# Kernel tuning notes

Hardware: AMD Instinct MI355X
Metric: run time of the kernel (lower is better)

## Reference

```python
import jax, jax.numpy as jnp
import numpy as np

NU, NI, E, D, B, L = 100000, 50000, 800000, 64, 1024, 2
P_DROP, TEMP = 0.25, 0.2
L1, L2, L3 = 0.2, 0.01, 1e-5


def setup_inputs() -> dict:
    k = jax.random.split(jax.random.key(0), 20)
    s = 0.02  # xavier-ish scale for embedding tables
    return dict(
        E_u_0=jax.random.normal(k[0], (NU, D), jnp.float32) * s,
        E_i_0=jax.random.normal(k[1], (NI, D), jnp.float32) * s,
        fuse_w=jax.random.normal(k[2], (E,), jnp.float32),
        fuse_b=jax.random.normal(k[3], (E,), jnp.float32),
        W1u=jax.random.normal(k[4], (D, D), jnp.float32) / np.sqrt(D),
        W1i=jax.random.normal(k[5], (D, D), jnp.float32) / np.sqrt(D),
        b1=jnp.zeros((D,), jnp.float32),
        W2=jax.random.normal(k[6], (D,), jnp.float32) / np.sqrt(D),
        b2=jnp.zeros((1,), jnp.float32),
        att_a=jax.random.normal(k[7], (2 * D,), jnp.float32) / np.sqrt(2 * D),
        wv_param=jax.random.normal(k[8], (E,), jnp.float32),
        Wg=jax.random.normal(k[9], (D, D), jnp.float32) / np.sqrt(D),
        adj_vals=jax.random.uniform(k[10], (E,), jnp.float32, 0.001, 0.02),
        drop_main_u=jax.random.uniform(k[11], (2 * L, E), jnp.float32),
        drop_aug_u=jax.random.uniform(k[12], (2 * L, E), jnp.float32),
        edge_src=jax.random.randint(k[13], (E,), 0, NU),
        edge_dst=jax.random.randint(k[14], (E,), 0, NI),
        uids=jax.random.randint(k[15], (B,), 0, NU),
        iids=jax.random.randint(k[16], (B,), 0, NI),
        pos_ids=jax.random.randint(k[17], (B,), 0, NI),
        neg_ids=jax.random.randint(k[18], (B,), 0, NI),
    )


def _forward(E_u_0, E_i_0, fuse_w, fuse_b, W1u, W1i, b1, W2, b2, att_a,
             wv_param, Wg, adj_vals, drop_main_u, drop_aug_u,
             edge_src, edge_dst, uids, iids, pos_ids, neg_ids):
    dt = adj_vals.dtype

    def spmm_u(vals, Xi):  # A @ Xi -> [NU, D]
        return jax.ops.segment_sum(vals[:, None] * Xi[edge_dst], edge_src, num_segments=NU)

    def spmm_i(vals, Xu):  # A.T @ Xu -> [NI, D]
        return jax.ops.segment_sum(vals[:, None] * Xu[edge_src], edge_dst, num_segments=NI)

    def mask(u):  # sparse_dropout: keep w.p. 1-p, rescale
        return (u > P_DROP).astype(dt) / (1.0 - P_DROP)

    def propagate(vals, drops):  # LightGCN-style sum over layers
        Eu, Ei = E_u_0, E_i_0
        Su, Si = Eu, Ei
        for layer in range(L):
            Eu_n = spmm_u(vals * mask(drops[2 * layer]), Ei)
            Ei_n = spmm_i(vals * mask(drops[2 * layer + 1]), Eu)
            Eu, Ei = Eu_n, Ei_n
            Su, Si = Su + Eu, Si + Ei
        return Su, Si

    E_u, E_i = propagate(adj_vals, drop_main_u)

    eu0, ei0 = E_u_0[edge_src], E_i_0[edge_dst]  # [E, D]
    # MLP view
    h = jax.nn.relu(eu0 @ W1u + ei0 @ W1i + b1)
    Ag_mlp = jax.nn.sigmoid(h @ W2 + b2[0])
    # WV view: learnable per-edge weight
    Ag_wv = jax.nn.sigmoid(wv_param)
    # GCN view: one propagation on current embeddings, bilinear edge score
    h_u = spmm_u(adj_vals, E_i)
    h_i = spmm_i(adj_vals, E_u)
    Ag_gcn = jax.nn.sigmoid(jnp.sum((h_u[edge_src] @ Wg) * h_i[edge_dst], axis=1))
    # ATT view: GAT-style
    Ag_att = jax.nn.sigmoid(jax.nn.leaky_relu(eu0 @ att_a[:D] + ei0 @ att_a[D:], 0.2))

    views = jnp.stack([Ag_mlp, Ag_wv, Ag_gcn, Ag_att])  # [4, E]
    w = jax.nn.softmax(jnp.tanh(fuse_w * views + fuse_b), axis=1)  # softmax over edges (as in source)
    Ag = jnp.sum(w * views, axis=0)
    Ag = (Ag + (views - Ag).sum(0)) / 5.0  # mlp_cof = 1 -> (sum(views) - 3*Ag) / 5

    # refine: sigmoid of endpoint dot products
    pre = jax.nn.sigmoid(jnp.sum(E_u[edge_src] * E_i[edge_dst], axis=1))
    baew = pre * Ag  # batch_aug_edge_weight

    aug_vals = jax.lax.stop_gradient(baew) * adj_vals  # new_graph * adj_norm (detach + Hadamard)
    Z_u, Z_i = propagate(aug_vals, drop_aug_u)

    # contrastive loss
    Gu, Gi = Z_u[uids], Z_i[iids]
    neg_sc = jnp.log(jnp.exp(Gu @ E_u.T / TEMP).sum(1) + 1e-8).mean() \
           + jnp.log(jnp.exp(Gi @ E_i.T / TEMP).sum(1) + 1e-8).mean()
    pos_sc = jnp.clip((Gu * E_u[uids]).sum(1) / TEMP, -5.0, 5.0).mean() \
           + jnp.clip((Gi * E_i[iids]).sum(1) / TEMP, -5.0, 5.0).mean()
    loss_cl = -pos_sc + neg_sc

    # BPR loss
    u_e, p_e, n_e = E_u[uids], E_i[pos_ids], E_i[neg_ids]
    diff = (u_e * p_e).sum(-1) - (u_e * n_e).sum(-1)
    loss_bpr = -jnp.log(jax.nn.sigmoid(diff)).mean()

    loss_pr = L2 * (-jnp.log(baew)).mean()

    params = [E_u_0, E_i_0, fuse_w, fuse_b, W1u, W1i, b1, W2, b2, att_a, wv_param, Wg]
    loss_reg = L3 * sum((p_ ** 2).sum() for p_ in params)

    loss = loss_bpr + L1 * loss_cl + loss_pr + loss_reg
    return loss, loss_bpr, L1 * loss_cl, loss_pr


def reference(E_u_0, E_i_0, fuse_w, fuse_b, W1u, W1i, b1, W2, b2, att_a,
              wv_param, Wg, adj_vals, drop_main_u, drop_aug_u,
              edge_src, edge_dst, uids, iids, pos_ids, neg_ids):
    return _forward(E_u_0, E_i_0, fuse_w, fuse_b, W1u, W1i, b1, W2, b2, att_a,
                    wv_param, Wg, adj_vals, drop_main_u, drop_aug_u,
                    edge_src, edge_dst, uids, iids, pos_ids, neg_ids)
```

## Files before the change

### kernel.cpp

```cpp
#include <hip/hip_runtime.h>
#include <math.h>

constexpr int NUc = 100000;
constexpr int NIc = 50000;
constexpr int Ec  = 800000;
constexpr int Bc  = 1024;

typedef __attribute__((ext_vector_type(8))) short short8;
typedef __attribute__((ext_vector_type(8))) unsigned short ushort8;
typedef __attribute__((ext_vector_type(4))) unsigned short ushort4v;
typedef __attribute__((ext_vector_type(4))) float floatx4;

__device__ __forceinline__ float sigf(float x) { return 1.f / (1.f + __expf(-x)); }
__device__ __forceinline__ float maskf(float u) { return (u > 0.25f) ? (1.f / 0.75f) : 0.f; }
__device__ __forceinline__ unsigned short f2bf(float f) {
    unsigned int u = __float_as_uint(f);
    unsigned int r = (u + 0x7fffu + ((u >> 16) & 1u)) >> 16;
    return (unsigned short)r;
}
__device__ __forceinline__ float bf2f(unsigned short u) {
    return __uint_as_float((unsigned int)u << 16);
}

__global__ void hist_k(const int* __restrict__ idx, int* __restrict__ cnt, int n) {
    int i = blockIdx.x * blockDim.x + threadIdx.x;
    if (i < n) atomicAdd(&cnt[idx[i]], 1);
}

__global__ void scan_block(const int* __restrict__ cnt, int* __restrict__ rp,
                           int* __restrict__ bsum, int N) {
    __shared__ int sh[1024];
    int i = blockIdx.x * 1024 + threadIdx.x;
    int v = (i < N) ? cnt[i] : 0;
    sh[threadIdx.x] = v;
    __syncthreads();
    for (int off = 1; off < 1024; off <<= 1) {
        int t = (threadIdx.x >= off) ? sh[threadIdx.x - off] : 0;
        __syncthreads();
        sh[threadIdx.x] += t;
        __syncthreads();
    }
    if (i < N) rp[i + 1] = sh[threadIdx.x];
    if (threadIdx.x == 1023) bsum[blockIdx.x] = sh[1023];
}

__global__ void scan_bsums(int* __restrict__ bsum, int nb) {
    __shared__ int sh[128];
    int t = threadIdx.x;
    int v = (t < nb) ? bsum[t] : 0;
    sh[t] = v;
    __syncthreads();
    for (int off = 1; off < 128; off <<= 1) {
        int x = (t >= off) ? sh[t - off] : 0;
        __syncthreads();
        sh[t] += x;
        __syncthreads();
    }
    if (t < nb) bsum[t] = sh[t] - v;
}

__global__ void scan_add(const int* __restrict__ bsum, int* __restrict__ rp, int N) {
    int i = blockIdx.x * blockDim.x + threadIdx.x;
    if (i == 0) rp[0] = 0;
    if (i < N) rp[i + 1] += bsum[i >> 10];
}

__global__ void fill_csr(const int* __restrict__ key, const int* __restrict__ other,
                         const float* __restrict__ adj, int* __restrict__ cur,
                         int* __restrict__ col, float* __restrict__ adjP,
                         int* __restrict__ pos, int n) {
    int i = blockIdx.x * blockDim.x + threadIdx.x;
    if (i < n) {
        int r = key[i];
        int p = atomicAdd(&cur[r], 1);
        col[p] = other[i];
        adjP[p] = adj[i];
        pos[i] = p;
    }
}

__global__ void build_rowu(const int* __restrict__ rp, int* __restrict__ rowu, int N) {
    int r = blockIdx.x * blockDim.x + threadIdx.x;
    if (r < N) {
        int s = rp[r], e = rp[r + 1];
        for (int p = s; p < e; ++p) rowu[p] = r;
    }
}

__global__ void build_wmain(const int* __restrict__ posu, const int* __restrict__ posi,
                            const float* __restrict__ adj, const float* __restrict__ dmain,
                            float* __restrict__ wMu0, float* __restrict__ wMu1,
                            float* __restrict__ wMi0, float* __restrict__ wMi1, int E) {
    int e = blockIdx.x * blockDim.x + threadIdx.x;
    if (e >= E) return;
    float a = adj[e];
    int pu = posu[e], pi = posi[e];
    wMu0[pu] = a * maskf(dmain[e]);
    wMi0[pi] = a * maskf(dmain[(size_t)Ec + e]);
    wMu1[pu] = a * maskf(dmain[2 * (size_t)Ec + e]);
    wMi1[pi] = a * maskf(dmain[3 * (size_t)Ec + e]);
}

__global__ void spmm_bf(const int* __restrict__ rp, const int* __restrict__ col,
                        const float* __restrict__ w, const unsigned short* __restrict__ Xbf,
                        float* __restrict__ Acc, const float* __restrict__ Base,
                        unsigned short* __restrict__ Ybf, int ystride, int yoff, int N) {
    int row = blockIdx.x * (blockDim.x >> 6) + (threadIdx.x >> 6);
    int lane = threadIdx.x & 63;
    if (row >= N) return;
    int s = rp[row], e = rp[row + 1];
    float acc = 0.f;
    int j = s;
    for (; j + 4 <= e; j += 4) {
        int c0 = col[j], c1 = col[j + 1], c2 = col[j + 2], c3 = col[j + 3];
        float w0 = w[j], w1 = w[j + 1], w2 = w[j + 2], w3 = w[j + 3];
        float x0 = bf2f(Xbf[(size_t)c0 * 64 + lane]);
        float x1 = bf2f(Xbf[(size_t)c1 * 64 + lane]);
        float x2 = bf2f(Xbf[(size_t)c2 * 64 + lane]);
        float x3 = bf2f(Xbf[(size_t)c3 * 64 + lane]);
        acc = fmaf(w0, x0, acc);
        acc = fmaf(w1, x1, acc);
        acc = fmaf(w2, x2, acc);
        acc = fmaf(w3, x3, acc);
    }
    for (; j < e; ++j) acc = fmaf(w[j], bf2f(Xbf[(size_t)col[j] * 64 + lane]), acc);
    size_t o = (size_t)row * 64 + lane;
    if (Acc) Acc[o] = (Base ? Base[o] : Acc[o]) + acc;
    if (Ybf) Ybf[(size_t)row * ystride + yoff + lane] = f2bf(acc);
}

__global__ void gemm_n64_bf(const unsigned short* __restrict__ Xbf, const float* __restrict__ W,
                            unsigned short* __restrict__ P, int ostride, int ooff, int N) {
    __shared__ float Wl[64 * 64];
    for (int i = threadIdx.x; i < 4096; i += blockDim.x) Wl[i] = W[i];
    __syncthreads();
    int wid = blockIdx.x * (blockDim.x >> 6) + (threadIdx.x >> 6);
    int lane = threadIdx.x & 63;
    for (int r = 0; r < 8; ++r) {
        int row = wid * 8 + r;
        if (row >= N) break;
        const unsigned short* xr = Xbf + (size_t)row * 64;
        float acc = 0.f;
#pragma unroll
        for (int k = 0; k < 64; ++k) acc = fmaf(bf2f(xr[k]), Wl[k * 64 + lane], acc);
        P[(size_t)row * ostride + ooff + lane] = f2bf(acc);
    }
}

__global__ void rowdot64(const float* __restrict__ X, const float* __restrict__ a,
                         float* __restrict__ out, int N) {
    int wid = blockIdx.x * (blockDim.x >> 6) + (threadIdx.x >> 6);
    int lane = threadIdx.x & 63;
    float av = a[lane];
    for (int r = 0; r < 8; ++r) {
        int row = wid * 8 + r;
        if (row >= N) break;
        float v = X[(size_t)row * 64 + lane] * av;
#pragma unroll
        for (int off = 32; off; off >>= 1) v += __shfl_xor(v, off, 64);
        if (lane == 0) out[row] = v;
    }
}

__global__ void cvt_bf16(const float4* __restrict__ X, ushort4* __restrict__ Y, int n4) {
    int i = blockIdx.x * blockDim.x + threadIdx.x;
    if (i < n4) {
        float4 v = X[i];
        Y[i] = make_ushort4(f2bf(v.x), f2bf(v.y), f2bf(v.z), f2bf(v.w));
    }
}

__global__ void cvt_pack4(const float4* __restrict__ X, unsigned short* __restrict__ P,
                          int ostride, int ooff, int N) {
    int t = blockIdx.x * blockDim.x + threadIdx.x;
    if (t >= N * 16) return;
    int node = t >> 4, q = t & 15;
    float4 v = X[t];
    ushort4* dst = (ushort4*)(P + (size_t)node * ostride + ooff);
    dst[q] = make_ushort4(f2bf(v.x), f2bf(v.y), f2bf(v.z), f2bf(v.w));
}

__global__ void pack_bf4(const ushort4* __restrict__ X, unsigned short* __restrict__ P,
                         int ostride, int ooff, int N) {
    int t = blockIdx.x * blockDim.x + threadIdx.x;
    if (t >= N * 16) return;
    int node = t >> 4, q = t & 15;
    ((ushort4*)(P + (size_t)node * ostride + ooff))[q] = X[t];
}

__global__ void __launch_bounds__(128) edge_pass1(
        const int* __restrict__ rowu, const int* __restrict__ colP,
        const unsigned short* __restrict__ PU, const unsigned short* __restrict__ PI,
        const float* __restrict__ b1, const float* __restrict__ W2,
        const float* __restrict__ b2,
        const float* __restrict__ auv, const float* __restrict__ aiv,
        float4* __restrict__ vp4, int E) {
    __shared__ ushort4v lds4[128 * 49];
    int p0 = blockIdx.x * 128;
    int tid = threadIdx.x;
#pragma unroll
    for (int it = 0; it < 24; ++it) {
        int flat = it * 128 + tid;
        int row = flat / 24, c = flat - row * 24;
        int d = colP[p0 + row];
        ushort8 g = *(const ushort8*)(PI + (size_t)d * 192 + c * 8);
        ushort4v lo = {g[0], g[1], g[2], g[3]};
        ushort4v hi = {g[4], g[5], g[6], g[7]};
        lds4[row * 49 + c * 2]     = lo;
        lds4[row * 49 + c * 2 + 1] = hi;
    }
    __syncthreads();
    int p = p0 + tid;
    int s = rowu[p];
    int d = colP[p];
    const ushort8* pu = (const ushort8*)(PU + (size_t)s * 192);
    const ushort4v* pl = lds4 + tid * 49;
    float r1 = 0.f, r2 = 0.f, r3 = 0.f;
#pragma unroll
    for (int k = 0; k < 8; ++k) {
        ushort8 u1 = pu[k], hu = pu[8 + k], su = pu[16 + k];
        ushort4v i1a = pl[2 * k], i1b = pl[2 * k + 1];
        ushort4v hia = pl[16 + 2 * k], hib = pl[16 + 2 * k + 1];
        ushort4v sia = pl[32 + 2 * k], sib = pl[32 + 2 * k + 1];
#pragma unroll
        for (int j = 0; j < 4; ++j) {
            float h = bf2f(u1[j]) + bf2f(i1a[j]) + b1[k * 8 + j];
            r1 = fmaf(fmaxf(h, 0.f), W2[k * 8 + j], r1);
            r2 = fmaf(bf2f(hu[j]), bf2f(hia[j]), r2);
            r3 = fmaf(bf2f(su[j]), bf2f(sia[j]), r3);
        }
#pragma unroll
        for (int j = 0; j < 4; ++j) {
            float h = bf2f(u1[4 + j]) + bf2f(i1b[j]) + b1[k * 8 + 4 + j];
            r1 = fmaf(fmaxf(h, 0.f), W2[k * 8 + 4 + j], r1);
            r2 = fmaf(bf2f(hu[4 + j]), bf2f(hib[j]), r2);
            r3 = fmaf(bf2f(su[4 + j]), bf2f(sib[j]), r3);
        }
    }
    float v0 = sigf(r1 + b2[0]);
    float v2 = sigf(r2);
    float ax = auv[s] + aiv[d];
    float v3 = sigf(ax > 0.f ? ax : 0.2f * ax);
    float pre = sigf(r3);
    vp4[p] = make_float4(v0, v2, v3, pre);
}

__global__ void edge_pass2a(const float4* __restrict__ vp4, const int* __restrict__ posu,
                            const float* __restrict__ fw, const float* __restrict__ fb,
                            const float* __restrict__ wv,
                            float4* __restrict__ viewsE, float* __restrict__ preE,
                            float* __restrict__ sumexp, int E) {
    int e = blockIdx.x * blockDim.x + threadIdx.x;
    float ex0 = 0.f, ex1 = 0.f, ex2 = 0.f, ex3 = 0.f;
    if (e < E) {
        float4 t = vp4[posu[e]];
        float v0 = t.x, v2 = t.y, v3 = t.z;
        float v1 = sigf(wv[e]);
        viewsE[e] = make_float4(v0, v1, v2, v3);
        preE[e] = t.w;
        float fwe = fw[e], fbe = fb[e];
        ex0 = __expf(tanhf(fmaf(fwe, v0, fbe)));
        ex1 = __expf(tanhf(fmaf(fwe, v1, fbe)));
        ex2 = __expf(tanhf(fmaf(fwe, v2, fbe)));
        ex3 = __expf(tanhf(fmaf(fwe, v3, fbe)));
    }
#pragma unroll
    for (int off = 32; off; off >>= 1) {
        ex0 += __shfl_xor(ex0, off, 64);
        ex1 += __shfl_xor(ex1, off, 64);
        ex2 += __shfl_xor(ex2, off, 64);
        ex3 += __shfl_xor(ex3, off, 64);
    }
    __shared__ float sh[4][4];
    int w = threadIdx.x >> 6;
    if ((threadIdx.x & 63) == 0) {
        sh[w][0] = ex0; sh[w][1] = ex1; sh[w][2] = ex2; sh[w][3] = ex3;
    }
    __syncthreads();
    if (threadIdx.x < 4)
        atomicAdd(&sumexp[threadIdx.x],
                  sh[0][threadIdx.x] + sh[1][threadIdx.x] + sh[2][threadIdx.x] + sh[3][threadIdx.x]);
}

__global__ void edge_pass2b(const float4* __restrict__ viewsE, const float* __restrict__ preE,
                            const float* __restrict__ fw, const float* __restrict__ fb,
                            const float* __restrict__ adj, const float* __restrict__ daug,
                            const int* __restrict__ posu, const int* __restrict__ posi,
                            const float* __restrict__ sumexp,
                            float* __restrict__ wAu0, float* __restrict__ wAu1,
                            float* __restrict__ wAi0, float* __restrict__ wAi1,
                            float* __restrict__ neglog, int E) {
    int e = blockIdx.x * blockDim.x + threadIdx.x;
    float nl = 0.f;
    if (e < E) {
        float s0 = sumexp[0], s1 = sumexp[1], s2 = sumexp[2], s3 = sumexp[3];
        float4 v = viewsE[e];
        float fwe = fw[e], fbe = fb[e];
        float w0 = __expf(tanhf(fmaf(fwe, v.x, fbe))) / s0;
        float w1 = __expf(tanhf(fmaf(fwe, v.y, fbe))) / s1;
        float w2 = __expf(tanhf(fmaf(fwe, v.z, fbe))) / s2;
        float w3 = __expf(tanhf(fmaf(fwe, v.w, fbe))) / s3;
        float agw = w0 * v.x + w1 * v.y + w2 * v.z + w3 * v.w;
        float sv = v.x + v.y + v.z + v.w;
        float Ag = (sv - 3.f * agw) * 0.2f;
        float bw = preE[e] * Ag;
        float av = bw * adj[e];
        int pu = posu[e], pi = posi[e];
        wAu0[pu] = av * maskf(daug[e]);
        wAi0[pi] = av * maskf(daug[(size_t)Ec + e]);
        wAu1[pu] = av * maskf(daug[2 * (size_t)Ec + e]);
        wAi1[pi] = av * maskf(daug[3 * (size_t)Ec + e]);
        nl = -logf(bw);
    }
#pragma unroll
    for (int off = 32; off; off >>= 1) nl += __shfl_xor(nl, off, 64);
    __shared__ float sh4[4];
    if ((threadIdx.x & 63) == 0) sh4[threadIdx.x >> 6] = nl;
    __syncthreads();
    if (threadIdx.x == 0) atomicAdd(neglog, sh4[0] + sh4[1] + sh4[2] + sh4[3]);
}

__global__ void gather_cvt(const float* __restrict__ X, const int* __restrict__ ids,
                           unsigned short* __restrict__ Y, int B_) {
    int t = blockIdx.x * blockDim.x + threadIdx.x;
    if (t >= B_ * 64) return;
    int b = t >> 6, k = t & 63;
    Y[t] = f2bf(X[(size_t)ids[b] * 64 + k]);
}

__global__ void lse_mfma(const unsigned short* __restrict__ Gbf,
                         const unsigned short* __restrict__ Ebf,
                         float* __restrict__ sums, int N, int tilesPerChunk) {
    int wid = blockIdx.x * (blockDim.x >> 6) + (threadIdx.x >> 6);
    int lane = threadIdx.x & 63;
    int bgroup = wid & 15;
    int chunk = wid >> 4;
    int ntiles = N >> 4;
    int t0 = chunk * tilesPerChunk;
    if (t0 >= ntiles) return;
    int t1 = t0 + tilesPerChunk; if (t1 > ntiles) t1 = ntiles;
    int m = lane & 15, quad = lane >> 4;

    short8 a0[4], a1[4];
#pragma unroll
    for (int t = 0; t < 4; ++t) {
        const short8* ap = (const short8*)(Gbf + ((size_t)(bgroup * 64 + t * 16 + m)) * 64 + quad * 8);
        a0[t] = ap[0];
        a1[t] = ap[4];
    }
    floatx4 rs[4];
#pragma unroll
    for (int t = 0; t < 4; ++t) rs[t] = (floatx4){0.f, 0.f, 0.f, 0.f};

    for (int jt = t0; jt < t1; ++jt) {
        const short8* bp = (const short8*)(Ebf + ((size_t)(jt * 16 + m)) * 64 + quad * 8);
        short8 bf0 = bp[0], bf1 = bp[4];
#pragma unroll
        for (int t = 0; t < 4; ++t) {
            floatx4 c = (floatx4){0.f, 0.f, 0.f, 0.f};
            c = __builtin_amdgcn_mfma_f32_16x16x32_bf16(a0[t], bf0, c, 0, 0, 0);
            c = __builtin_amdgcn_mfma_f32_16x16x32_bf16(a1[t], bf1, c, 0, 0, 0);
#pragma unroll
            for (int r = 0; r < 4; ++r) rs[t][r] += __expf(c[r] * 5.f);
        }
    }
#pragma unroll
    for (int t = 0; t < 4; ++t) {
#pragma unroll
        for (int r = 0; r < 4; ++r) {
            float v = rs[t][r];
            v += __shfl_xor(v, 1, 64);
            v += __shfl_xor(v, 2, 64);
            v += __shfl_xor(v, 4, 64);
            v += __shfl_xor(v, 8, 64);
            if (m == 0) atomicAdd(&sums[bgroup * 64 + t * 16 + quad * 4 + r], v);
        }
    }
}

__global__ void sumsq(const float* __restrict__ x, int n, float* __restrict__ acc) {
    float s = 0.f;
    for (int i = blockIdx.x * blockDim.x + threadIdx.x; i < n; i += gridDim.x * blockDim.x) {
        float v = x[i];
        s = fmaf(v, v, s);
    }
#pragma unroll
    for (int off = 32; off; off >>= 1) s += __shfl_xor(s, off, 64);
    __shared__ float sh[4];
    if ((threadIdx.x & 63) == 0) sh[threadIdx.x >> 6] = s;
    __syncthreads();
    if (threadIdx.x == 0) atomicAdd(acc, sh[0] + sh[1] + sh[2] + sh[3]);
}

__global__ void finalize_kernel(const float* __restrict__ sumexp_u, const float* __restrict__ sumexp_i,
                                const float* __restrict__ Su, const float* __restrict__ Si,
                                const float* __restrict__ Zu, const float* __restrict__ Zi,
                                const int* __restrict__ uids, const int* __restrict__ iids,
                                const int* __restrict__ pids, const int* __restrict__ nids,
                                const float* __restrict__ neglog, const float* __restrict__ regsum,
                                float* __restrict__ out) {
    int b = threadIdx.x;
    float lse = logf(sumexp_u[b] + 1e-8f) + logf(sumexp_i[b] + 1e-8f);
    int u = uids[b], ii = iids[b], p = pids[b], n = nids[b];
    const float* zu = Zu + (size_t)u * 64;
    const float* su = Su + (size_t)u * 64;
    const float* zi = Zi + (size_t)ii * 64;
    const float* si = Si + (size_t)ii * 64;
    const float* pe = Si + (size_t)p * 64;
    const float* ne = Si + (size_t)n * 64;
    float du = 0.f, di = 0.f, dp = 0.f, dn = 0.f;
#pragma unroll
    for (int k = 0; k < 64; ++k) {
        du = fmaf(zu[k], su[k], du);
        di = fmaf(zi[k], si[k], di);
        dp = fmaf(su[k], pe[k], dp);
        dn = fmaf(su[k], ne[k], dn);
    }
    float pos = fminf(fmaxf(du * 5.f, -5.f), 5.f) + fminf(fmaxf(di * 5.f, -5.f), 5.f);
    float diff = dp - dn;
    float bpr = log1pf(__expf(-diff));
#pragma unroll
    for (int off = 32; off; off >>= 1) {
        lse += __shfl_xor(lse, off, 64);
        pos += __shfl_xor(pos, off, 64);
        bpr += __shfl_xor(bpr, off, 64);
    }
    __shared__ float sl[16], sp[16], sb[16];
    int w = b >> 6;
    if ((b & 63) == 0) { sl[w] = lse; sp[w] = pos; sb[w] = bpr; }
    __syncthreads();
    if (b == 0) {
        float L = 0.f, P = 0.f, Bz = 0.f;
        for (int i = 0; i < 16; ++i) { L += sl[i]; P += sp[i]; Bz += sb[i]; }
        float neg_sc = L * (1.f / Bc);
        float pos_sc = P * (1.f / Bc);
        float loss_cl = neg_sc - pos_sc;
        float l1cl = 0.2f * loss_cl;
        float loss_bpr = Bz * (1.f / Bc);
        float loss_pr = 0.01f * (neglog[0] * (1.f / Ec));
        float loss_reg = 1e-5f * regsum[0];
        out[0] = loss_bpr + l1cl + loss_pr + loss_reg;
        out[1] = loss_bpr;
        out[2] = l1cl;
        out[3] = loss_pr;
    }
}

extern "C" void kernel_launch(void* const* d_in, const int* in_sizes, int n_in,
                              void* d_out, int out_size, void* d_ws, size_t ws_size,
                              hipStream_t stream) {
    const float* Eu0    = (const float*)d_in[0];
    const float* Ei0    = (const float*)d_in[1];
    const float* fuse_w = (const float*)d_in[2];
    const float* fuse_b = (const float*)d_in[3];
    const float* W1u    = (const float*)d_in[4];
    const float* W1i    = (const float*)d_in[5];
    const float* b1     = (const float*)d_in[6];
    const float* W2     = (const float*)d_in[7];
    const float* b2     = (const float*)d_in[8];
    const float* att    = (const float*)d_in[9];
    const float* wv     = (const float*)d_in[10];
    const float* Wg     = (const float*)d_in[11];
    const float* adj    = (const float*)d_in[12];
    const float* dmain  = (const float*)d_in[13];
    const float* daug   = (const float*)d_in[14];
    const int*   esrc   = (const int*)d_in[15];
    const int*   edst   = (const int*)d_in[16];
    const int*   uids   = (const int*)d_in[17];
    const int*   iids   = (const int*)d_in[18];
    const int*   pids   = (const int*)d_in[19];
    const int*   nids   = (const int*)d_in[20];
    float* out = (float*)d_out;

    char* base = (char*)d_ws;
    size_t off = 0;
    auto alloc = [&](size_t bytes) -> char* {
        char* pp = base + off;
        off = (off + bytes + 255) & ~(size_t)255;
        return pp;
    };
    float* Su   = (float*)alloc((size_t)NUc * 64 * 4);
    float* Si   = (float*)alloc((size_t)NIc * 64 * 4);
    char* blkZ = alloc((size_t)NUc * 64 * 4 + (size_t)NIc * 64 * 4);
    unsigned short* PU = (unsigned short*)blkZ;
    float4* viewsE = (float4*)blkZ;
    float* preE   = (float*)(blkZ + (size_t)Ec * 16);
    float* Zu = (float*)blkZ;
    float* Zi = (float*)(blkZ + (size_t)NUc * 64 * 4);
    float4* vp4 = (float4*)alloc((size_t)Ec * 16);
    unsigned short* Eu0bf = (unsigned short*)alloc((size_t)NUc * 64 * 2);
    unsigned short* Ei0bf = (unsigned short*)alloc((size_t)NIc * 64 * 2);
    unsigned short* Subf  = (unsigned short*)alloc((size_t)NUc * 64 * 2);
    unsigned short* Sibf  = (unsigned short*)alloc((size_t)NIc * 64 * 2);
    unsigned short* Bubf  = (unsigned short*)alloc((size_t)NUc * 64 * 2);
    unsigned short* Bibf  = (unsigned short*)alloc((size_t)NIc * 64 * 2);
    unsigned short* hubf  = (unsigned short*)alloc((size_t)NUc * 64 * 2);
    unsigned short* hibf  = (unsigned short*)alloc((size_t)NIc * 64 * 2);
    char* blkA = alloc((size_t)Ec * 4 * 6);
    float* adjPu = (float*)blkA;
    float* adjPi = (float*)(blkA + (size_t)Ec * 4);
    float* wAu0  = (float*)(blkA + (size_t)Ec * 8);
    float* wAu1  = (float*)(blkA + (size_t)Ec * 12);
    float* wAi0  = (float*)(blkA + (size_t)Ec * 16);
    float* wAi1  = (float*)(blkA + (size_t)Ec * 20);
    unsigned short* PI = (unsigned short*)blkA;
    float* wMu0  = (float*)alloc((size_t)Ec * 4);
    float* wMu1  = (float*)alloc((size_t)Ec * 4);
    float* wMi0  = (float*)alloc((size_t)Ec * 4);
    float* wMi1  = (float*)alloc((size_t)Ec * 4);
    float* auv  = (float*)alloc((size_t)NUc * 4);
    float* aiv  = (float*)alloc((size_t)NIc * 4);
    int* rowu  = (int*)alloc((size_t)Ec * 4);
    unsigned short* Gubf = (unsigned short*)alloc((size_t)Bc * 64 * 2);
    unsigned short* Gibf = (unsigned short*)alloc((size_t)Bc * 64 * 2);
    float* sumexp4 = (float*)alloc(4 * 4);
    float* neglog  = (float*)alloc(4);
    float* regsum  = (float*)alloc(4);
    float* sumexp_u= (float*)alloc((size_t)Bc * 4);
    float* sumexp_i= (float*)alloc((size_t)Bc * 4);
    int* rpu   = (int*)alloc((size_t)(NUc + 1) * 4);
    int* rpi   = (int*)alloc((size_t)(NIc + 1) * 4);
    int* colu  = (int*)alloc((size_t)Ec * 4);
    int* coli  = (int*)alloc((size_t)Ec * 4);
    int* posu  = (int*)alloc((size_t)Ec * 4);
    int* posi  = (int*)alloc((size_t)Ec * 4);
    int* cnt   = (int*)alloc((size_t)NUc * 4);
    int* cur   = (int*)alloc((size_t)NUc * 4);
    int* bsum  = (int*)alloc(128 * 4);

    dim3 b256(256);
    const int nbU = (NUc + 1023) / 1024;
    const int nbI = (NIc + 1023) / 1024;
    const dim3 gE((Ec + 255) / 256);
    const dim3 gU((NUc + 3) / 4), gI((NIc + 3) / 4);
    const dim3 gU8((NUc + 31) / 32), gI8((NIc + 31) / 32);
    const dim3 gUp((NUc * 16 + 255) / 256), gIp((NIc * 16 + 255) / 256);

    hipMemsetAsync(cnt, 0, (size_t)NUc * 4, stream);
    hist_k<<<gE, b256, 0, stream>>>(esrc, cnt, Ec);
    scan_block<<<dim3(nbU), dim3(1024), 0, stream>>>(cnt, rpu, bsum, NUc);
    scan_bsums<<<dim3(1), dim3(128), 0, stream>>>(bsum, nbU);
    scan_add<<<dim3((NUc + 255) / 256), b256, 0, stream>>>(bsum, rpu, NUc);
    hipMemcpyAsync(cur, rpu, (size_t)NUc * 4, hipMemcpyDeviceToDevice, stream);
    fill_csr<<<gE, b256, 0, stream>>>(esrc, edst, adj, cur, colu, adjPu, posu, Ec);
    build_rowu<<<dim3((NUc + 255) / 256), b256, 0, stream>>>(rpu, rowu, NUc);

    hipMemsetAsync(cnt, 0, (size_t)NIc * 4, stream);
    hist_k<<<gE, b256, 0, stream>>>(edst, cnt, Ec);
    scan_block<<<dim3(nbI), dim3(1024), 0, stream>>>(cnt, rpi, bsum, NIc);
    scan_bsums<<<dim3(1), dim3(128), 0, stream>>>(bsum, nbI);
    scan_add<<<dim3((NIc + 255) / 256), b256, 0, stream>>>(bsum, rpi, NIc);
    hipMemcpyAsync(cur, rpi, (size_t)NIc * 4, hipMemcpyDeviceToDevice, stream);
    fill_csr<<<gE, b256, 0, stream>>>(edst, esrc, adj, cur, coli, adjPi, posi, Ec);

    build_wmain<<<gE, b256, 0, stream>>>(posu, posi, adj, dmain, wMu0, wMu1, wMi0, wMi1, Ec);

    cvt_bf16<<<gUp, b256, 0, stream>>>((const float4*)Eu0, (ushort4*)Eu0bf, NUc * 16);
    cvt_bf16<<<gIp, b256, 0, stream>>>((const float4*)Ei0, (ushort4*)Ei0bf, NIc * 16);

    spmm_bf<<<gU, b256, 0, stream>>>(rpu, colu, wMu0, Ei0bf, Su, Eu0, Bubf, 64, 0, NUc);
    spmm_bf<<<gI, b256, 0, stream>>>(rpi, coli, wMi0, Eu0bf, Si, Ei0, Bibf, 64, 0, NIc);
    spmm_bf<<<gU, b256, 0, stream>>>(rpu, colu, wMu1, Bibf, Su, nullptr, nullptr, 64, 0, NUc);
    spmm_bf<<<gI, b256, 0, stream>>>(rpi, coli, wMi1, Bubf, Si, nullptr, nullptr, 64, 0, NIc);

    cvt_bf16<<<gUp, b256, 0, stream>>>((const float4*)Su, (ushort4*)Subf, NUc * 16);
    cvt_bf16<<<gIp, b256, 0, stream>>>((const float4*)Si, (ushort4*)Sibf, NIc * 16);

    spmm_bf<<<gU, b256, 0, stream>>>(rpu, colu, adjPu, Sibf, nullptr, nullptr, hubf, 64, 0, NUc);
    spmm_bf<<<gI, b256, 0, stream>>>(rpi, coli, adjPi, Subf, nullptr, nullptr, hibf, 64, 0, NIc);
    gemm_n64_bf<<<gU8, b256, 0, stream>>>(hubf, Wg, PU, 192, 64, NUc);
    gemm_n64_bf<<<gU8, b256, 0, stream>>>(Eu0bf, W1u, PU, 192, 0, NUc);
    gemm_n64_bf<<<gI8, b256, 0, stream>>>(Ei0bf, W1i, PI, 192, 0, NIc);
    pack_bf4<<<gIp, b256, 0, stream>>>((const ushort4*)hibf, PI, 192, 64, NIc);
    cvt_pack4<<<gUp, b256, 0, stream>>>((const float4*)Su, PU, 192, 128, NUc);
    cvt_pack4<<<gIp, b256, 0, stream>>>((const float4*)Si, PI, 192, 128, NIc);

    rowdot64<<<gU8, b256, 0, stream>>>(Eu0, att, auv, NUc);
    rowdot64<<<gI8, b256, 0, stream>>>(Ei0, att + 64, aiv, NIc);

    edge_pass1<<<dim3(Ec / 128), dim3(128), 0, stream>>>(
        rowu, colu, PU, PI, b1, W2, b2, auv, aiv, vp4, Ec);

    hipMemsetAsync(sumexp4, 0, 4 * 4, stream);
    edge_pass2a<<<gE, b256, 0, stream>>>(vp4, posu, fuse_w, fuse_b, wv,
                                         viewsE, preE, sumexp4, Ec);

    hipMemsetAsync(neglog, 0, 4, stream);
    edge_pass2b<<<gE, b256, 0, stream>>>(
        viewsE, preE, fuse_w, fuse_b, adj, daug, posu, posi, sumexp4,
        wAu0, wAu1, wAi0, wAi1, neglog, Ec);

    spmm_bf<<<gU, b256, 0, stream>>>(rpu, colu, wAu0, Ei0bf, Zu, Eu0, Bubf, 64, 0, NUc);
    spmm_bf<<<gI, b256, 0, stream>>>(rpi, coli, wAi0, Eu0bf, Zi, Ei0, Bibf, 64, 0, NIc);
    spmm_bf<<<gU, b256, 0, stream>>>(rpu, colu, wAu1, Bibf, Zu, nullptr, nullptr, 64, 0, NUc);
    spmm_bf<<<gI, b256, 0, stream>>>(rpi, coli, wAi1, Bubf, Zi, nullptr, nullptr, 64, 0, NIc);

    gather_cvt<<<dim3((Bc * 64 + 255) / 256), b256, 0, stream>>>(Zu, uids, Gubf, Bc);
    gather_cvt<<<dim3((Bc * 64 + 255) / 256), b256, 0, stream>>>(Zi, iids, Gibf, Bc);
    hipMemsetAsync(sumexp_u, 0, (size_t)Bc * 4, stream);
    hipMemsetAsync(sumexp_i, 0, (size_t)Bc * 4, stream);
    lse_mfma<<<dim3(640), b256, 0, stream>>>(Gubf, Subf, sumexp_u, NUc, 40);
    lse_mfma<<<dim3(320), b256, 0, stream>>>(Gibf, Sibf, sumexp_i, NIc, 40);

    hipMemsetAsync(regsum, 0, 4, stream);
    auto ss = [&](const float* p, int n) {
        int g = (n + 2047) / 2048;
        if (g > 1024) g = 1024;
        if (g < 1) g = 1;
        sumsq<<<dim3(g), b256, 0, stream>>>(p, n, regsum);
    };
    ss(Eu0, NUc * 64); ss(Ei0, NIc * 64); ss(fuse_w, Ec); ss(fuse_b, Ec);
    ss(W1u, 4096); ss(W1i, 4096); ss(b1, 64); ss(W2, 64); ss(b2, 1);
    ss(att, 128); ss(wv, Ec); ss(Wg, 4096);

    finalize_kernel<<<dim3(1), dim3(1024), 0, stream>>>(
        sumexp_u, sumexp_i, Su, Si, Zu, Zi, uids, iids, pids, nids, neglog, regsum, out);
}
```

Before: 1.390 ms.

## Replace scattered edge-weight writes with permutation gathers and parallelize batch dot products

The CSR fill now records a permutation from CSR position to original edge. Main and augmented edge-weight arrays are built by gathering through that permutation, so the old random scatter writes via posu/posi become coalesced writes with random reads. The batch dot products formerly done serially per thread in the single-block finalize kernel move to a wave-per-sample kernel with shuffle reductions. This adds extra kernel launches, an extra intermediate array and some re-reading of the mask arrays.

```diff
diff --git a/kernel.cpp b/kernel.cpp
--- a/kernel.cpp
+++ b/kernel.cpp
@@ -66,16 +66,15 @@
 }
 
 __global__ void fill_csr(const int* __restrict__ key, const int* __restrict__ other,
-                         const float* __restrict__ adj, int* __restrict__ cur,
-                         int* __restrict__ col, float* __restrict__ adjP,
-                         int* __restrict__ pos, int n) {
+                         int* __restrict__ cur, int* __restrict__ col,
+                         int* __restrict__ pos, int* __restrict__ perm, int n) {
     int i = blockIdx.x * blockDim.x + threadIdx.x;
     if (i < n) {
         int r = key[i];
         int p = atomicAdd(&cur[r], 1);
         col[p] = other[i];
-        adjP[p] = adj[i];
         pos[i] = p;
+        perm[p] = i;
     }
 }
 
@@ -87,18 +86,22 @@
     }
 }
 
-__global__ void build_wmain(const int* __restrict__ posu, const int* __restrict__ posi,
-                            const float* __restrict__ adj, const float* __restrict__ dmain,
-                            float* __restrict__ wMu0, float* __restrict__ wMu1,
-                            float* __restrict__ wMi0, float* __restrict__ wMi1, int E) {
-    int e = blockIdx.x * blockDim.x + threadIdx.x;
-    if (e >= E) return;
-    float a = adj[e];
-    int pu = posu[e], pi = posi[e];
-    wMu0[pu] = a * maskf(dmain[e]);
-    wMi0[pi] = a * maskf(dmain[(size_t)Ec + e]);
-    wMu1[pu] = a * maskf(dmain[2 * (size_t)Ec + e]);
-    wMi1[pi] = a * maskf(dmain[3 * (size_t)Ec + e]);
+__global__ void build_w_gather(const int* __restrict__ perm, const float* __restrict__ vals,
+                               const float* __restrict__ dA, const float* __restrict__ dB,
+                               float* __restrict__ outA, float* __restrict__ outB, int E) {
+    int p = blockIdx.x * blockDim.x + threadIdx.x;
+    if (p >= E) return;
+    int e = perm[p];
+    float a = vals[e];
+    outA[p] = a * maskf(dA[e]);
+    outB[p] = a * maskf(dB[e]);
+}
+
+__global__ void gather_vals(const int* __restrict__ perm, const float* __restrict__ vals,
+                            float* __restrict__ outA, int E) {
+    int p = blockIdx.x * blockDim.x + threadIdx.x;
+    if (p >= E) return;
+    outA[p] = vals[perm[p]];
 }
 
 __global__ void spmm_bf(const int* __restrict__ rp, const int* __restrict__ col,
@@ -284,12 +287,8 @@
 
 __global__ void edge_pass2b(const float4* __restrict__ viewsE, const float* __restrict__ preE,
                             const float* __restrict__ fw, const float* __restrict__ fb,
-                            const float* __restrict__ adj, const float* __restrict__ daug,
-                            const int* __restrict__ posu, const int* __restrict__ posi,
-                            const float* __restrict__ sumexp,
-                            float* __restrict__ wAu0, float* __restrict__ wAu1,
-                            float* __restrict__ wAi0, float* __restrict__ wAi1,
-                            float* __restrict__ neglog, int E) {
+                            const float* __restrict__ adj, const float* __restrict__ sumexp,
+                            float* __restrict__ av, float* __restrict__ neglog, int E) {
     int e = blockIdx.x * blockDim.x + threadIdx.x;
     float nl = 0.f;
     if (e < E) {
@@ -304,12 +303,7 @@
         float sv = v.x + v.y + v.z + v.w;
         float Ag = (sv - 3.f * agw) * 0.2f;
         float bw = preE[e] * Ag;
-        float av = bw * adj[e];
-        int pu = posu[e], pi = posi[e];
-        wAu0[pu] = av * maskf(daug[e]);
-        wAi0[pi] = av * maskf(daug[(size_t)Ec + e]);
-        wAu1[pu] = av * maskf(daug[2 * (size_t)Ec + e]);
-        wAi1[pi] = av * maskf(daug[3 * (size_t)Ec + e]);
+        av[e] = bw * adj[e];
         nl = -logf(bw);
     }
 #pragma unroll
@@ -392,33 +386,40 @@
     if (threadIdx.x == 0) atomicAdd(acc, sh[0] + sh[1] + sh[2] + sh[3]);
 }
 
+__global__ void batch_partial(const float* __restrict__ Su, const float* __restrict__ Si,
+                              const float* __restrict__ Zu, const float* __restrict__ Zi,
+                              const int* __restrict__ uids, const int* __restrict__ iids,
+                              const int* __restrict__ pids, const int* __restrict__ nids,
+                              float* __restrict__ pos_b, float* __restrict__ bpr_b) {
+    int b = blockIdx.x * (blockDim.x >> 6) + (threadIdx.x >> 6);
+    if (b >= Bc) return;
+    int lane = threadIdx.x & 63;
+    int u = uids[b], ii = iids[b], p = pids[b], n = nids[b];
+    float zu = Zu[(size_t)u * 64 + lane],  su = Su[(size_t)u * 64 + lane];
+    float zi = Zi[(size_t)ii * 64 + lane], si = Si[(size_t)ii * 64 + lane];
+    float pe = Si[(size_t)p * 64 + lane],  ne = Si[(size_t)n * 64 + lane];
+    float du = zu * su, di = zi * si, dp = su * pe, dn = su * ne;
+#pragma unroll
+    for (int off = 32; off; off >>= 1) {
+        du += __shfl_xor(du, off, 64);
+        di += __shfl_xor(di, off, 64);
+        dp += __shfl_xor(dp, off, 64);
+        dn += __shfl_xor(dn, off, 64);
+    }
+    if (lane == 0) {
+        pos_b[b] = fminf(fmaxf(du * 5.f, -5.f), 5.f) + fminf(fmaxf(di * 5.f, -5.f), 5.f);
+        bpr_b[b] = log1pf(__expf(-(dp - dn)));
+    }
+}
+
 __global__ void finalize_kernel(const float* __restrict__ sumexp_u, const float* __restrict__ sumexp_i,
-                                const float* __restrict__ Su, const float* __restrict__ Si,
-                                const float* __restrict__ Zu, const float* __restrict__ Zi,
-                                const int* __restrict__ uids, const int* __restrict__ iids,
-                                const int* __restrict__ pids, const int* __restrict__ nids,
+                                const float* __restrict__ pos_b, const float* __restrict__ bpr_b,
                                 const float* __restrict__ neglog, const float* __restrict__ regsum,
                                 float* __restrict__ out) {
     int b = threadIdx.x;
     float lse = logf(sumexp_u[b] + 1e-8f) + logf(sumexp_i[b] + 1e-8f);
-    int u = uids[b], ii = iids[b], p = pids[b], n = nids[b];
-    const float* zu = Zu + (size_t)u * 64;
-    const float* su = Su + (size_t)u * 64;
-    const float* zi = Zi + (size_t)ii * 64;
-    const float* si = Si + (size_t)ii * 64;
-    const float* pe = Si + (size_t)p * 64;
-    const float* ne = Si + (size_t)n * 64;
-    float du = 0.f, di = 0.f, dp = 0.f, dn = 0.f;
-#pragma unroll
-    for (int k = 0; k < 64; ++k) {
-        du = fmaf(zu[k], su[k], du);
-        di = fmaf(zi[k], si[k], di);
-        dp = fmaf(su[k], pe[k], dp);
-        dn = fmaf(su[k], ne[k], dn);
-    }
-    float pos = fminf(fmaxf(du * 5.f, -5.f), 5.f) + fminf(fmaxf(di * 5.f, -5.f), 5.f);
-    float diff = dp - dn;
-    float bpr = log1pf(__expf(-diff));
+    float pos = pos_b[b];
+    float bpr = bpr_b[b];
 #pragma unroll
     for (int off = 32; off; off >>= 1) {
         lse += __shfl_xor(lse, off, 64);
@@ -508,6 +509,7 @@
     float* wMu1  = (float*)alloc((size_t)Ec * 4);
     float* wMi0  = (float*)alloc((size_t)Ec * 4);
     float* wMi1  = (float*)alloc((size_t)Ec * 4);
+    float* av    = (float*)alloc((size_t)Ec * 4);
     float* auv  = (float*)alloc((size_t)NUc * 4);
     float* aiv  = (float*)alloc((size_t)NIc * 4);
     int* rowu  = (int*)alloc((size_t)Ec * 4);
@@ -518,12 +520,16 @@
     float* regsum  = (float*)alloc(4);
     float* sumexp_u= (float*)alloc((size_t)Bc * 4);
     float* sumexp_i= (float*)alloc((size_t)Bc * 4);
+    float* pos_b   = (float*)alloc((size_t)Bc * 4);
+    float* bpr_b   = (float*)alloc((size_t)Bc * 4);
     int* rpu   = (int*)alloc((size_t)(NUc + 1) * 4);
     int* rpi   = (int*)alloc((size_t)(NIc + 1) * 4);
     int* colu  = (int*)alloc((size_t)Ec * 4);
     int* coli  = (int*)alloc((size_t)Ec * 4);
     int* posu  = (int*)alloc((size_t)Ec * 4);
     int* posi  = (int*)alloc((size_t)Ec * 4);
+    int* permu = (int*)alloc((size_t)Ec * 4);
+    int* permi = (int*)alloc((size_t)Ec * 4);
     int* cnt   = (int*)alloc((size_t)NUc * 4);
     int* cur   = (int*)alloc((size_t)NUc * 4);
     int* bsum  = (int*)alloc(128 * 4);
@@ -542,7 +548,7 @@
     scan_bsums<<<dim3(1), dim3(128), 0, stream>>>(bsum, nbU);
     scan_add<<<dim3((NUc + 255) / 256), b256, 0, stream>>>(bsum, rpu, NUc);
     hipMemcpyAsync(cur, rpu, (size_t)NUc * 4, hipMemcpyDeviceToDevice, stream);
-    fill_csr<<<gE, b256, 0, stream>>>(esrc, edst, adj, cur, colu, adjPu, posu, Ec);
+    fill_csr<<<gE, b256, 0, stream>>>(esrc, edst, cur, colu, posu, permu, Ec);
     build_rowu<<<dim3((NUc + 255) / 256), b256, 0, stream>>>(rpu, rowu, NUc);
 
     hipMemsetAsync(cnt, 0, (size_t)NIc * 4, stream);
@@ -551,9 +557,12 @@
     scan_bsums<<<dim3(1), dim3(128), 0, stream>>>(bsum, nbI);
     scan_add<<<dim3((NIc + 255) / 256), b256, 0, stream>>>(bsum, rpi, NIc);
     hipMemcpyAsync(cur, rpi, (size_t)NIc * 4, hipMemcpyDeviceToDevice, stream);
-    fill_csr<<<gE, b256, 0, stream>>>(edst, esrc, adj, cur, coli, adjPi, posi, Ec);
-
-    build_wmain<<<gE, b256, 0, stream>>>(posu, posi, adj, dmain, wMu0, wMu1, wMi0, wMi1, Ec);
+    fill_csr<<<gE, b256, 0, stream>>>(edst, esrc, cur, coli, posi, permi, Ec);
+
+    build_w_gather<<<gE, b256, 0, stream>>>(permu, adj, dmain, dmain + 2 * (size_t)Ec, wMu0, wMu1, Ec);
+    build_w_gather<<<gE, b256, 0, stream>>>(permi, adj, dmain + (size_t)Ec, dmain + 3 * (size_t)Ec, wMi0, wMi1, Ec);
+    gather_vals<<<gE, b256, 0, stream>>>(permu, adj, adjPu, Ec);
+    gather_vals<<<gE, b256, 0, stream>>>(permi, adj, adjPi, Ec);
 
     cvt_bf16<<<gUp, b256, 0, stream>>>((const float4*)Eu0, (ushort4*)Eu0bf, NUc * 16);
     cvt_bf16<<<gIp, b256, 0, stream>>>((const float4*)Ei0, (ushort4*)Ei0bf, NIc * 16);
@@ -587,8 +596,10 @@
 
     hipMemsetAsync(neglog, 0, 4, stream);
     edge_pass2b<<<gE, b256, 0, stream>>>(
-        viewsE, preE, fuse_w, fuse_b, adj, daug, posu, posi, sumexp4,
-        wAu0, wAu1, wAi0, wAi1, neglog, Ec);
+        viewsE, preE, fuse_w, fuse_b, adj, sumexp4, av, neglog, Ec);
+
+    build_w_gather<<<gE, b256, 0, stream>>>(permu, av, daug, daug + 2 * (size_t)Ec, wAu0, wAu1, Ec);
+    build_w_gather<<<gE, b256, 0, stream>>>(permi, av, daug + (size_t)Ec, daug + 3 * (size_t)Ec, wAi0, wAi1, Ec);
 
     spmm_bf<<<gU, b256, 0, stream>>>(rpu, colu, wAu0, Ei0bf, Zu, Eu0, Bubf, 64, 0, NUc);
     spmm_bf<<<gI, b256, 0, stream>>>(rpi, coli, wAi0, Eu0bf, Zi, Ei0, Bibf, 64, 0, NIc);
@@ -601,6 +612,9 @@
     hipMemsetAsync(sumexp_i, 0, (size_t)Bc * 4, stream);
     lse_mfma<<<dim3(640), b256, 0, stream>>>(Gubf, Subf, sumexp_u, NUc, 40);
     lse_mfma<<<dim3(320), b256, 0, stream>>>(Gibf, Sibf, sumexp_i, NIc, 40);
+
+    batch_partial<<<dim3(Bc / 4), b256, 0, stream>>>(Su, Si, Zu, Zi, uids, iids, pids, nids,
+                                                     pos_b, bpr_b);
 
     hipMemsetAsync(regsum, 0, 4, stream);
     auto ss = [&](const float* p, int n) {
@@ -614,5 +628,5 @@
     ss(att, 128); ss(wv, Ec); ss(Wg, 4096);
 
     finalize_kernel<<<dim3(1), dim3(1024), 0, stream>>>(
-        sumexp_u, sumexp_i, Su, Si, Zu, Zi, uids, iids, pids, nids, neglog, regsum, out);
-}
+        sumexp_u, sumexp_i, pos_b, bpr_b, neglog, regsum, out);
+}
```

Result: no change. 1.368 ms (-1.6%).
